# Performance work log

Hardware: AMD Instinct MI355X
Metric: run time of the kernel (lower is better)

Reference implementation:

```python
import jax, jax.numpy as jnp
import numpy as np
from jax import lax

B, T, K = 64, 2048, 128


def setup_inputs() -> dict:
    key = jax.random.key(0)
    k0, k1, k2, k3, k4, k5 = jax.random.split(key, 6)
    emissions = jax.random.normal(k0, (B, T, K), dtype=jnp.float32)
    lengths = jax.random.randint(k1, (B,), T // 2, T + 1)
    mask = jnp.arange(T)[None, :] < lengths[:, None]  # left-aligned [B,T] bool
    target = jax.random.bernoulli(k2, 0.5, (B, T, K))  # supervision set [B,T,K] bool
    forbidden_transitions = jax.random.bernoulli(k3, 0.1, (K, K))
    transitions = jax.random.normal(k4, (K, K), dtype=jnp.float32) * 0.01
    start_transitions = jax.random.normal(k5, (K,), dtype=jnp.float32) * 0.01
    return dict(emissions=emissions, mask=mask, target=target,
                transitions=transitions, start_transitions=start_transitions,
                forbidden_transitions=forbidden_transitions)


def reference(emissions, mask, target, transitions, start_transitions, forbidden_transitions):
    # Faithful to torch forward: transitions masked with -10000; end_transitions unused;
    # raw (unmasked) start_transitions added to EVERY timestep (as in the source).
    trans = jnp.where(forbidden_transitions, jnp.float32(-10000.0), transitions)  # [K,K]
    sup_em = jnp.where(target, emissions, jnp.float32(-100000.0))  # masked_fill(~target)
    bi = jnp.concatenate([sup_em, emissions], axis=0)  # [2B,T,K]
    bi = bi + start_transitions  # broadcast over all timesteps (source quirk)

    alpha0 = bi[:, 0]  # [2B,K]

    def step(alpha, em_t):
        # logdotexp: logsumexp_i(alpha[:,i] + trans[i,j]) + em_t[:,j]
        new = jax.nn.logsumexp(alpha[:, :, None] + trans[None, :, :], axis=1) + em_t
        return new, new

    _, outs = lax.scan(step, alpha0, jnp.swapaxes(bi[:, 1:], 0, 1))  # [T-1,2B,K]
    outs = jnp.concatenate([alpha0[None], outs], axis=0)  # [T,2B,K]

    lengths = mask.sum(-1)  # [B]
    last = jnp.concatenate([lengths, lengths]) - 1  # [2B]
    z_alpha = outs[last, jnp.arange(2 * B)]  # alpha at last valid step, [2B,K]
    z = jax.nn.logsumexp(z_alpha, axis=-1)  # [2B]
    supervised_z = z[:B]
    unsupervised_z = z[B:]
    return supervised_z - unsupervised_z
```

## Files before the change

### kernel.cpp

```cpp
#include <hip/hip_runtime.h>
#include <stdint.h>

#define BB 64
#define TT 2048
#define KK 128
#define CH 32

typedef float f32x16 __attribute__((ext_vector_type(16)));
typedef float f32x2  __attribute__((ext_vector_type(2)));

__device__ __forceinline__ float waveMax(float v) {
#pragma unroll
    for (int off = 32; off; off >>= 1) v = fmaxf(v, __shfl_xor(v, off, 64));
    return v;
}
__device__ __forceinline__ float waveSum(float v) {
#pragma unroll
    for (int off = 32; off; off >>= 1) v += __shfl_xor(v, off, 64);
    return v;
}
__device__ __forceinline__ int waveSumI(int v) {
#pragma unroll
    for (int off = 32; off; off >>= 1) v += __shfl_xor(v, off, 64);
    return v;
}
__device__ __forceinline__ float quadSum(float s) {
    int x = __builtin_amdgcn_mov_dpp(__float_as_int(s), 0xB1, 0xf, 0xf, true);
    s += __int_as_float(x);
    x = __builtin_amdgcn_mov_dpp(__float_as_int(s), 0x4E, 0xf, 0xf, true);
    s += __int_as_float(x);
    return s;
}
__device__ __forceinline__ float waveMaxFast(float v) {
    int x = __builtin_amdgcn_mov_dpp(__float_as_int(v), 0xB1, 0xf, 0xf, true);
    v = fmaxf(v, __int_as_float(x));
    x = __builtin_amdgcn_mov_dpp(__float_as_int(v), 0x4E, 0xf, 0xf, true);
    v = fmaxf(v, __int_as_float(x));
#pragma unroll
    for (int off = 4; off <= 32; off <<= 1) v = fmaxf(v, __shfl_xor(v, off, 64));
    return v;
}

template<int C> __device__ __forceinline__ float dppMax(float v) {
    int x = __builtin_amdgcn_mov_dpp(__float_as_int(v), C, 0xf, 0xf, true);
    return fmaxf(v, __int_as_float(x));
}
__device__ __forceinline__ float waveMaxTo63(float v) {
    v = dppMax<0xB1>(v);
    v = dppMax<0x4E>(v);
    v = dppMax<0x124>(v);
    v = dppMax<0x128>(v);
    v = dppMax<0x142>(v);
    v = dppMax<0x143>(v);
    return v;
}

__device__ __forceinline__ void lds_barrier() {
    asm volatile("s_waitcnt lgkmcnt(0)\n\ts_barrier" ::: "memory");
}

#define PKFMA(ep, wp, acc) acc = __builtin_elementwise_fma(ep, wp, acc)

#define MATVEC_QUARTER(Wa, Wb, ev, sOut) {                          \
    const float4 e0 = ev[0], e1 = ev[1], e2 = ev[2], e3 = ev[3];    \
    const float4 e4 = ev[4], e5 = ev[5], e6 = ev[6], e7 = ev[7];    \
    f32x2 a0 = {0.f,0.f}, a1 = {0.f,0.f}, a2 = {0.f,0.f}, a3 = {0.f,0.f}; \
    PKFMA(((f32x2){e0.x, e0.y}), ((f32x2){Wa[0],  Wa[1]}),  a0);    \
    PKFMA(((f32x2){e0.z, e0.w}), ((f32x2){Wa[2],  Wa[3]}),  a1);    \
    PKFMA(((f32x2){e1.x, e1.y}), ((f32x2){Wa[4],  Wa[5]}),  a2);    \
    PKFMA(((f32x2){e1.z, e1.w}), ((f32x2){Wa[6],  Wa[7]}),  a3);    \
    PKFMA(((f32x2){e2.x, e2.y}), ((f32x2){Wa[8],  Wa[9]}),  a0);    \
    PKFMA(((f32x2){e2.z, e2.w}), ((f32x2){Wa[10], Wa[11]}), a1);    \
    PKFMA(((f32x2){e3.x, e3.y}), ((f32x2){Wa[12], Wa[13]}), a2);    \
    PKFMA(((f32x2){e3.z, e3.w}), ((f32x2){Wa[14], Wa[15]}), a3);    \
    PKFMA(((f32x2){e4.x, e4.y}), ((f32x2){Wb[0],  Wb[1]}),  a0);    \
    PKFMA(((f32x2){e4.z, e4.w}), ((f32x2){Wb[2],  Wb[3]}),  a1);    \
    PKFMA(((f32x2){e5.x, e5.y}), ((f32x2){Wb[4],  Wb[5]}),  a2);    \
    PKFMA(((f32x2){e5.z, e5.w}), ((f32x2){Wb[6],  Wb[7]}),  a3);    \
    PKFMA(((f32x2){e6.x, e6.y}), ((f32x2){Wb[8],  Wb[9]}),  a0);    \
    PKFMA(((f32x2){e6.z, e6.w}), ((f32x2){Wb[10], Wb[11]}), a1);    \
    PKFMA(((f32x2){e7.x, e7.y}), ((f32x2){Wb[12], Wb[13]}), a2);    \
    PKFMA(((f32x2){e7.z, e7.w}), ((f32x2){Wb[14], Wb[15]}), a3);    \
    const f32x2 s2 = (a0 + a1) + (a2 + a3);                         \
    sOut = s2[0] + s2[1]; }

#define W_LIST(X) \
    X(0)  X(1)  X(2)  X(3)  X(4)  X(5)  X(6)  X(7)  \
    X(8)  X(9)  X(10) X(11) X(12) X(13) X(14) X(15) \
    X(16) X(17) X(18) X(19) X(20) X(21) X(22) X(23) \
    X(24) X(25) X(26) X(27) X(28) X(29) X(30) X(31) \
    X(32) X(33) X(34) X(35) X(36) X(37) X(38) X(39) \
    X(40) X(41) X(42) X(43) X(44) X(45) X(46) X(47) \
    X(48) X(49) X(50) X(51) X(52) X(53) X(54) X(55) \
    X(56) X(57) X(58) X(59) X(60) X(61) X(62) X(63)

#define WDECL(j) f32x2 W_##j;
#define WINIT_F(j) W_##j = (f32x2){ \
    forb[(2*(j)  )*KK + k] ? 0.0f : __expf(trans[(2*(j)  )*KK + k]), \
    forb[(2*(j)+1)*KK + k] ? 0.0f : __expf(trans[(2*(j)+1)*KK + k]) };
#define WINIT_B(j) W_##j = (f32x2){ \
    forb[k*KK + 2*(j)  ] ? 0.0f : __expf(trans[k*KK + 2*(j)  ]), \
    forb[k*KK + 2*(j)+1] ? 0.0f : __expf(trans[k*KK + 2*(j)+1]) };
#define WPIN(j) asm volatile("" : "+a"(W_##j));
#define WFMA(j, p0, p1, A0, A1) { const float4 E = ev[(j)]; \
    PKFMA(((f32x2){E.x, E.y}), W_##p0, A0); \
    PKFMA(((f32x2){E.z, E.w}), W_##p1, A1); }

extern "C" __global__ __launch_bounds__(128, 1)
__attribute__((amdgpu_waves_per_eu(1, 1)))
void crf_fb_kernel(const float* __restrict__ em,
                   const int* __restrict__ mask,
                   const int* __restrict__ tgt,
                   const float* __restrict__ trans,
                   const float* __restrict__ start,
                   const int* __restrict__ forb,
                   float* __restrict__ ef,
                   float* __restrict__ db,
                   float* __restrict__ Mfb)
{
    const int tid  = threadIdx.x;
    const int k    = tid;
    const int w    = tid >> 6;
    const int lane = tid & 63;
    const bool fwdDir = (blockIdx.x < 2 * BB);
    const int c    = blockIdx.x & (2 * BB - 1);
    const int b    = c & (BB - 1);
    const bool sup = (c < BB);

    __shared__ __align__(16) float biLDS[2][CH][KK];
    __shared__ __align__(16) float eLDS[2][KK];
    __shared__ __align__(8)  float wmLDS[2];
    __shared__ float redLDS[2];
    __shared__ int lenLDS;

    if (tid == 0) lenLDS = 0;
    int ps = 0;
    const int4* __restrict__ mrow = (const int4*)(mask + (size_t)b * TT);
#pragma unroll
    for (int it = 0; it < 4; ++it) {
        const int4 m4 = mrow[tid + 128 * it];
        ps += m4.x + m4.y + m4.z + m4.w;
    }
    ps = waveSumI(ps);
    __syncthreads();
    if (lane == 0) atomicAdd(&lenLDS, ps);

    const float st = start[k];
    const float* __restrict__ emrow = em + (size_t)b * TT * KK;
    const int* __restrict__ trow = tgt + (size_t)b * TT * KK;

    W_LIST(WDECL)
    if (fwdDir) {
        W_LIST(WINIT_F)
    } else {
        W_LIST(WINIT_B)
    }
    W_LIST(WPIN)
    __syncthreads();
    const int len = lenLDS;
    const int mid = len >> 1;
    const int N   = fwdDir ? mid : (len - 1 - mid);
    const int t0  = fwdDir ? 0 : (len - 1);

    float v0 = emrow[(size_t)t0 * KK + k];
    if (sup && !trow[(size_t)t0 * KK + k]) v0 = -100000.0f;
    v0 += st;
    const float wm0 = waveMax(v0);
    if (lane == 0) redLDS[w] = wm0;
    __syncthreads();
    const float M0 = fmaxf(redLDS[0], redLDS[1]);
    double M = (double)M0;
    float eNew = __expf(v0 - M0);
    eLDS[0][k] = eNew;

    const int scol = (tid & 31) << 2;
    const float4 stc = *(const float4*)(start + scol);
    auto stageChunk = [&](int bf, int m) {
        const int base_n = 1 + CH * m;
        const int t_base = fwdDir ? base_n : (len - base_n - CH);
#pragma unroll
        for (int i = 0; i < 8; ++i) {
            const int row = (tid >> 5) + (i << 2);
            const int t = t_base + row;
            float4 e4 = *(const float4*)(emrow + (size_t)t * KK + scol);
            if (sup) {
                const int4 t4 = *(const int4*)(trow + (size_t)t * KK + scol);
                e4.x = t4.x ? e4.x : -100000.0f;
                e4.y = t4.y ? e4.y : -100000.0f;
                e4.z = t4.z ? e4.z : -100000.0f;
                e4.w = t4.w ? e4.w : -100000.0f;
            }
            e4.x += stc.x; e4.y += stc.y; e4.z += stc.z; e4.w += stc.w;
            *(float4*)&biLDS[bf][row][scol] = e4;
        }
    };

    const int nChunks = (N + CH - 1) / CH;
    int buf = 0;
    stageChunk(0, 0);
    lds_barrier();

    for (int m = 0; m < nChunks; ++m) {
        if (m + 1 < nChunks) stageChunk(buf ^ 1, m + 1);
        const int base_n = 1 + CH * m;
        const int rem = N - base_n + 1;
        const int lim = rem < CH ? rem : CH;
#pragma unroll 4
        for (int i = 0; i < lim; ++i) {
            const int n = base_n + i;
            const int p = (n - 1) & 1;

            const int pos = fwdDir ? i : (CH - 1 - i);
            float bi = biLDS[buf][pos][k];
            if (!fwdDir && n == N) bi = 0.0f;

            if ((n & 3) == 3) {
                const float u = waveMaxTo63(__logf(eNew));
                if (lane == 63) wmLDS[w] = u;
            }
            float r = 0.0f;
            if ((n & 3) == 0) {
                const float2 wmv = *(const float2*)wmLDS;
                r = fmaxf(wmv.x, wmv.y);
                M += (double)r;
            }
            const float f = __expf(bi - r);

            const float4* __restrict__ ev = (const float4*)eLDS[p];
            f32x2 a0 = {0.f,0.f}, a1 = {0.f,0.f}, a2 = {0.f,0.f}, a3 = {0.f,0.f};
            WFMA( 0,  0,  1, a0, a1) WFMA( 1,  2,  3, a2, a3)
            WFMA( 2,  4,  5, a0, a1) WFMA( 3,  6,  7, a2, a3)
            WFMA( 4,  8,  9, a0, a1) WFMA( 5, 10, 11, a2, a3)
            WFMA( 6, 12, 13, a0, a1) WFMA( 7, 14, 15, a2, a3)
            WFMA( 8, 16, 17, a0, a1) WFMA( 9, 18, 19, a2, a3)
            WFMA(10, 20, 21, a0, a1) WFMA(11, 22, 23, a2, a3)
            WFMA(12, 24, 25, a0, a1) WFMA(13, 26, 27, a2, a3)
            WFMA(14, 28, 29, a0, a1) WFMA(15, 30, 31, a2, a3)
            WFMA(16, 32, 33, a0, a1) WFMA(17, 34, 35, a2, a3)
            WFMA(18, 36, 37, a0, a1) WFMA(19, 38, 39, a2, a3)
            WFMA(20, 40, 41, a0, a1) WFMA(21, 42, 43, a2, a3)
            WFMA(22, 44, 45, a0, a1) WFMA(23, 46, 47, a2, a3)
            WFMA(24, 48, 49, a0, a1) WFMA(25, 50, 51, a2, a3)
            WFMA(26, 52, 53, a0, a1) WFMA(27, 54, 55, a2, a3)
            WFMA(28, 56, 57, a0, a1) WFMA(29, 58, 59, a2, a3)
            WFMA(30, 60, 61, a0, a1) WFMA(31, 62, 63, a2, a3)
            const f32x2 aa = (a0 + a1) + (a2 + a3);
            const float s = aa[0] + aa[1];

            eNew = s * f;
            eLDS[p ^ 1][k] = eNew;

            lds_barrier();
        }
        buf ^= 1;
    }

    (fwdDir ? ef : db)[(size_t)c * KK + k] = eNew;
    if (tid == 0) Mfb[(fwdDir ? 0 : 2 * BB) + c] = (float)M;
}

extern "C" __global__ void crf_combine_kernel(const float* __restrict__ ef,
                                              const float* __restrict__ db,
                                              const float* __restrict__ Mfb,
                                              float* __restrict__ out)
{
    const int b = blockIdx.x;
    const int tid = threadIdx.x;
    const int wv = tid >> 6, lane = tid & 63;
    __shared__ float red[2][2];
    __shared__ float z[2];
#pragma unroll
    for (int s = 0; s < 2; ++s) {
        const int c = b + s * BB;
        const float v = ef[(size_t)c * KK + tid] * db[(size_t)c * KK + tid];
        const float p = waveSum(v);
        if (lane == 0) red[s][wv] = p;
    }
    __syncthreads();
    if (tid < 2) {
        const int c = b + tid * BB;
        z[tid] = Mfb[c] + Mfb[2 * BB + c] + __logf(red[tid][0] + red[tid][1]);
    }
    __syncthreads();
    if (tid == 0) out[b] = z[0] - z[1];
}

extern "C" __global__ __launch_bounds__(512)
__attribute__((amdgpu_waves_per_eu(2, 2)))
void crf_chain_kernel(const float* __restrict__ em, const int* __restrict__ mask,
                      const int* __restrict__ tgt, const float* __restrict__ trans,
                      const float* __restrict__ start, const int* __restrict__ forb,
                      float* __restrict__ zbuf)
{
    const int tid = threadIdx.x;
    const int k = tid >> 2, q = tid & 3, w = tid >> 6, lane = tid & 63;
    const int c = blockIdx.x, b = c & (BB - 1);
    const bool sup = (c < BB);
    __shared__ __align__(16) float eLDS[2][KK];
    __shared__ float wmLDS[8];
    __shared__ float redLDS[8];
    __shared__ int lenLDS;
    if (tid == 0) lenLDS = 0;
    const int4 m4 = ((const int4*)(mask + (size_t)b * TT))[tid];
    int ps = m4.x + m4.y + m4.z + m4.w;
    ps = waveSumI(ps);
    __syncthreads();
    if (lane == 0) atomicAdd(&lenLDS, ps);
    const float st = start[k];
    const float* __restrict__ emrow = em + (size_t)b * TT * KK;
    const int* __restrict__ trow = tgt + (size_t)b * TT * KK;
    const int ib = q * 32;
    f32x16 Wa, Wb;
#pragma unroll
    for (int j = 0; j < 16; ++j) {
        Wa[j] = forb[(ib + j     ) * KK + k] ? 0.0f : __expf(trans[(ib + j     ) * KK + k]);
        Wb[j] = forb[(ib + 16 + j) * KK + k] ? 0.0f : __expf(trans[(ib + 16 + j) * KK + k]);
    }
    float v0 = emrow[k];
    if (sup && !trow[k]) v0 = -100000.0f;
    v0 += st;
    const float wm0 = waveMax(v0);
    if (lane == 0) redLDS[w] = wm0;
    __syncthreads();
    const int len = lenLDS;
    float M0 = fmaxf(fmaxf(fmaxf(redLDS[0], redLDS[1]), fmaxf(redLDS[2], redLDS[3])),
                     fmaxf(fmaxf(redLDS[4], redLDS[5]), fmaxf(redLDS[6], redLDS[7])));
    double M = (double)M0;
    float eNew = __expf(v0 - M0);
    if (q == 0) eLDS[0][k] = eNew;
    auto bival = [&](int t) -> float {
        float e0 = emrow[(size_t)t * KK + k];
        if (sup) { if (!trow[(size_t)t * KK + k]) e0 = -100000.0f; }
        return e0 + st;
    };
    float biA = (len > 1) ? bival(1) : 0.0f;
    float biB = (len > 2) ? bival(2) : 0.0f;
    float biC = (len > 3) ? bival(3) : 0.0f;
    float biD = (len > 4) ? bival(4) : 0.0f;
    float sPrev = 1.0f, baPrev = 0.0f;
    lds_barrier();
#pragma unroll 4
    for (int t = 1; t < len; ++t) {
        const int p = (t - 1) & 1;
        const float biN = (t + 4 < len) ? bival(t + 4) : 0.0f;
        if ((t & 3) == 3) {
            const float u = __logf(sPrev) + baPrev;
            const float wmx = waveMaxFast(u);
            if (lane == 0) wmLDS[w] = wmx;
        }
        float r = 0.0f;
        if ((t & 3) == 0) {
            r = fmaxf(fmaxf(fmaxf(wmLDS[0], wmLDS[1]), fmaxf(wmLDS[2], wmLDS[3])),
                      fmaxf(fmaxf(wmLDS[4], wmLDS[5]), fmaxf(wmLDS[6], wmLDS[7])));
            M += (double)r;
        }
        const float ba = biA - r;
        const float f = __expf(ba);
        const float4* __restrict__ ev = (const float4*)eLDS[p] + q * 8;
        float s;
        MATVEC_QUARTER(Wa, Wb, ev, s)
        s = quadSum(s);
        eNew = s * f;
        if (q == 0) eLDS[p ^ 1][k] = eNew;
        sPrev = s; baPrev = ba;
        biA = biB; biB = biC; biC = biD; biD = biN;
        lds_barrier();
    }
    const float sm = waveSum((q == 0) ? eNew : 0.0f);
    if (lane == 0) redLDS[w] = sm;
    __syncthreads();
    if (tid == 0) {
        const float ss = ((redLDS[0] + redLDS[1]) + (redLDS[2] + redLDS[3]))
                       + ((redLDS[4] + redLDS[5]) + (redLDS[6] + redLDS[7]));
        zbuf[c] = (float)(M + (double)__logf(ss));
    }
}

extern "C" __global__ void crf_final_kernel(const float* __restrict__ z,
                                            float* __restrict__ out)
{
    const int b = threadIdx.x;
    out[b] = z[b] - z[b + BB];
}

extern "C" void kernel_launch(void* const* d_in, const int* in_sizes, int n_in,
                              void* d_out, int out_size, void* d_ws, size_t ws_size,
                              hipStream_t stream) {
    const float* em    = (const float*)d_in[0];
    const int*   mask  = (const int*)d_in[1];
    const int*   tgt   = (const int*)d_in[2];
    const float* trans = (const float*)d_in[3];
    const float* start = (const float*)d_in[4];
    const int*   forb  = (const int*)d_in[5];

    const size_t need = (size_t)(2 * 2 * BB * KK + 4 * BB) * sizeof(float);
    if (ws_size >= need) {
        float* ef  = (float*)d_ws;
        float* db  = ef + 2 * BB * KK;
        float* Mfb = db + 2 * BB * KK;
        crf_fb_kernel<<<4 * BB, 128, 0, stream>>>(em, mask, tgt, trans, start,
                                                  forb, ef, db, Mfb);
        crf_combine_kernel<<<BB, 128, 0, stream>>>(ef, db, Mfb, (float*)d_out);
    } else {
        float* zbuf = (float*)d_ws;
        crf_chain_kernel<<<2 * BB, 512, 0, stream>>>(em, mask, tgt, trans, start,
                                                     forb, zbuf);
        crf_final_kernel<<<1, BB, 0, stream>>>(zbuf, (float*)d_out);
    }
}
```

Baseline: 819.1 us.

## Run each CRF chain in a single wave with two states per lane

The forward/backward chain kernel drops from two waves to a single 64-lane wave per block, with each lane owning two consecutive states and holding both transition columns pinned in AGPRs. Within one wave the per-step barriers and the cross-wave LDS max exchange can go: the running max is computed with an in-wave DPP/shuffle reduction and the new alphas are written to and read from LDS by the same wave. In exchange each lane now does twice the packed FMAs per step on the serial critical path and uses roughly twice the register storage for weights. The chunk loop also has its unroll factors retuned.

```diff
diff --git a/kernel.cpp b/kernel.cpp
--- a/kernel.cpp
+++ b/kernel.cpp
@@ -38,20 +38,6 @@
     v = fmaxf(v, __int_as_float(x));
 #pragma unroll
     for (int off = 4; off <= 32; off <<= 1) v = fmaxf(v, __shfl_xor(v, off, 64));
-    return v;
-}
-
-template<int C> __device__ __forceinline__ float dppMax(float v) {
-    int x = __builtin_amdgcn_mov_dpp(__float_as_int(v), C, 0xf, 0xf, true);
-    return fmaxf(v, __int_as_float(x));
-}
-__device__ __forceinline__ float waveMaxTo63(float v) {
-    v = dppMax<0xB1>(v);
-    v = dppMax<0x4E>(v);
-    v = dppMax<0x124>(v);
-    v = dppMax<0x128>(v);
-    v = dppMax<0x142>(v);
-    v = dppMax<0x143>(v);
     return v;
 }
 
@@ -94,19 +80,26 @@
     X(48) X(49) X(50) X(51) X(52) X(53) X(54) X(55) \
     X(56) X(57) X(58) X(59) X(60) X(61) X(62) X(63)
 
-#define WDECL(j) f32x2 W_##j;
-#define WINIT_F(j) W_##j = (f32x2){ \
-    forb[(2*(j)  )*KK + k] ? 0.0f : __expf(trans[(2*(j)  )*KK + k]), \
-    forb[(2*(j)+1)*KK + k] ? 0.0f : __expf(trans[(2*(j)+1)*KK + k]) };
-#define WINIT_B(j) W_##j = (f32x2){ \
-    forb[k*KK + 2*(j)  ] ? 0.0f : __expf(trans[k*KK + 2*(j)  ]), \
-    forb[k*KK + 2*(j)+1] ? 0.0f : __expf(trans[k*KK + 2*(j)+1]) };
-#define WPIN(j) asm volatile("" : "+a"(W_##j));
-#define WFMA(j, p0, p1, A0, A1) { const float4 E = ev[(j)]; \
-    PKFMA(((f32x2){E.x, E.y}), W_##p0, A0); \
-    PKFMA(((f32x2){E.z, E.w}), W_##p1, A1); }
-
-extern "C" __global__ __launch_bounds__(128, 1)
+#define WDECL(j) f32x2 WA_##j, WB_##j;
+#define WINITPIN_F(j) \
+    WA_##j = (f32x2){ forb[(2*(j)  )*KK + k0] ? 0.0f : __expf(trans[(2*(j)  )*KK + k0]), \
+                      forb[(2*(j)+1)*KK + k0] ? 0.0f : __expf(trans[(2*(j)+1)*KK + k0]) }; \
+    WB_##j = (f32x2){ forb[(2*(j)  )*KK + k1] ? 0.0f : __expf(trans[(2*(j)  )*KK + k1]), \
+                      forb[(2*(j)+1)*KK + k1] ? 0.0f : __expf(trans[(2*(j)+1)*KK + k1]) }; \
+    asm volatile("" : "+a"(WA_##j), "+a"(WB_##j));
+#define WINITPIN_B(j) \
+    WA_##j = (f32x2){ forb[k0*KK + 2*(j)  ] ? 0.0f : __expf(trans[k0*KK + 2*(j)  ]), \
+                      forb[k0*KK + 2*(j)+1] ? 0.0f : __expf(trans[k0*KK + 2*(j)+1]) }; \
+    WB_##j = (f32x2){ forb[k1*KK + 2*(j)  ] ? 0.0f : __expf(trans[k1*KK + 2*(j)  ]), \
+                      forb[k1*KK + 2*(j)+1] ? 0.0f : __expf(trans[k1*KK + 2*(j)+1]) }; \
+    asm volatile("" : "+a"(WA_##j), "+a"(WB_##j));
+#define WF(j, a, b) { const float4 E = ev[(j)]; \
+    PKFMA(((f32x2){E.x, E.y}), WA_##a, A0); \
+    PKFMA(((f32x2){E.z, E.w}), WA_##b, A0b); \
+    PKFMA(((f32x2){E.x, E.y}), WB_##a, A1); \
+    PKFMA(((f32x2){E.z, E.w}), WB_##b, A1b); }
+
+extern "C" __global__ __launch_bounds__(64, 1)
 __attribute__((amdgpu_waves_per_eu(1, 1)))
 void crf_fb_kernel(const float* __restrict__ em,
                    const int* __restrict__ mask,
@@ -118,10 +111,9 @@
                    float* __restrict__ db,
                    float* __restrict__ Mfb)
 {
-    const int tid  = threadIdx.x;
-    const int k    = tid;
-    const int w    = tid >> 6;
-    const int lane = tid & 63;
+    const int lane = threadIdx.x;
+    const int k0   = lane << 1;
+    const int k1   = k0 + 1;
     const bool fwdDir = (blockIdx.x < 2 * BB);
     const int c    = blockIdx.x & (2 * BB - 1);
     const int b    = c & (BB - 1);
@@ -129,58 +121,52 @@
 
     __shared__ __align__(16) float biLDS[2][CH][KK];
     __shared__ __align__(16) float eLDS[2][KK];
-    __shared__ __align__(8)  float wmLDS[2];
-    __shared__ float redLDS[2];
-    __shared__ int lenLDS;
-
-    if (tid == 0) lenLDS = 0;
+
     int ps = 0;
     const int4* __restrict__ mrow = (const int4*)(mask + (size_t)b * TT);
 #pragma unroll
-    for (int it = 0; it < 4; ++it) {
-        const int4 m4 = mrow[tid + 128 * it];
+    for (int it = 0; it < 8; ++it) {
+        const int4 m4 = mrow[lane + 64 * it];
         ps += m4.x + m4.y + m4.z + m4.w;
     }
-    ps = waveSumI(ps);
-    __syncthreads();
-    if (lane == 0) atomicAdd(&lenLDS, ps);
-
-    const float st = start[k];
+    const int len = waveSumI(ps);
+
     const float* __restrict__ emrow = em + (size_t)b * TT * KK;
     const int* __restrict__ trow = tgt + (size_t)b * TT * KK;
 
     W_LIST(WDECL)
     if (fwdDir) {
-        W_LIST(WINIT_F)
+        W_LIST(WINITPIN_F)
     } else {
-        W_LIST(WINIT_B)
-    }
-    W_LIST(WPIN)
-    __syncthreads();
-    const int len = lenLDS;
+        W_LIST(WINITPIN_B)
+    }
+
     const int mid = len >> 1;
     const int N   = fwdDir ? mid : (len - 1 - mid);
     const int t0  = fwdDir ? 0 : (len - 1);
 
-    float v0 = emrow[(size_t)t0 * KK + k];
-    if (sup && !trow[(size_t)t0 * KK + k]) v0 = -100000.0f;
-    v0 += st;
-    const float wm0 = waveMax(v0);
-    if (lane == 0) redLDS[w] = wm0;
-    __syncthreads();
-    const float M0 = fmaxf(redLDS[0], redLDS[1]);
+    float2 v0 = *(const float2*)(emrow + (size_t)t0 * KK + k0);
+    if (sup) {
+        const int2 t2 = *(const int2*)(trow + (size_t)t0 * KK + k0);
+        v0.x = t2.x ? v0.x : -100000.0f;
+        v0.y = t2.y ? v0.y : -100000.0f;
+    }
+    const float2 st2 = *(const float2*)(start + k0);
+    v0.x += st2.x; v0.y += st2.y;
+    const float M0 = waveMaxFast(fmaxf(v0.x, v0.y));
     double M = (double)M0;
-    float eNew = __expf(v0 - M0);
-    eLDS[0][k] = eNew;
-
-    const int scol = (tid & 31) << 2;
+    float eNew0 = __expf(v0.x - M0);
+    float eNew1 = __expf(v0.y - M0);
+    *(f32x2*)&eLDS[0][k0] = (f32x2){eNew0, eNew1};
+
+    const int scol = (lane & 31) << 2;
     const float4 stc = *(const float4*)(start + scol);
     auto stageChunk = [&](int bf, int m) {
         const int base_n = 1 + CH * m;
         const int t_base = fwdDir ? base_n : (len - base_n - CH);
-#pragma unroll
-        for (int i = 0; i < 8; ++i) {
-            const int row = (tid >> 5) + (i << 2);
+#pragma unroll 4
+        for (int pss = 0; pss < 16; ++pss) {
+            const int row = (pss << 1) + (lane >> 5);
             const int t = t_base + row;
             float4 e4 = *(const float4*)(emrow + (size_t)t * KK + scol);
             if (sup) {
@@ -198,65 +184,53 @@
     const int nChunks = (N + CH - 1) / CH;
     int buf = 0;
     stageChunk(0, 0);
-    lds_barrier();
+    float rPend = 0.0f;
 
     for (int m = 0; m < nChunks; ++m) {
         if (m + 1 < nChunks) stageChunk(buf ^ 1, m + 1);
         const int base_n = 1 + CH * m;
         const int rem = N - base_n + 1;
         const int lim = rem < CH ? rem : CH;
-#pragma unroll 4
+#pragma unroll 2
         for (int i = 0; i < lim; ++i) {
             const int n = base_n + i;
             const int p = (n - 1) & 1;
-
             const int pos = fwdDir ? i : (CH - 1 - i);
-            float bi = biLDS[buf][pos][k];
-            if (!fwdDir && n == N) bi = 0.0f;
+
+            float2 bi = *(const float2*)&biLDS[buf][pos][k0];
+            if (!fwdDir && n == N) { bi.x = 0.0f; bi.y = 0.0f; }
 
             if ((n & 3) == 3) {
-                const float u = waveMaxTo63(__logf(eNew));
-                if (lane == 63) wmLDS[w] = u;
+                rPend = waveMaxFast(__logf(fmaxf(eNew0, eNew1)));
             }
             float r = 0.0f;
-            if ((n & 3) == 0) {
-                const float2 wmv = *(const float2*)wmLDS;
-                r = fmaxf(wmv.x, wmv.y);
-                M += (double)r;
-            }
-            const float f = __expf(bi - r);
+            if ((n & 3) == 0) { r = rPend; M += (double)r; }
+            const float f0 = __expf(bi.x - r);
+            const float f1 = __expf(bi.y - r);
 
             const float4* __restrict__ ev = (const float4*)eLDS[p];
-            f32x2 a0 = {0.f,0.f}, a1 = {0.f,0.f}, a2 = {0.f,0.f}, a3 = {0.f,0.f};
-            WFMA( 0,  0,  1, a0, a1) WFMA( 1,  2,  3, a2, a3)
-            WFMA( 2,  4,  5, a0, a1) WFMA( 3,  6,  7, a2, a3)
-            WFMA( 4,  8,  9, a0, a1) WFMA( 5, 10, 11, a2, a3)
-            WFMA( 6, 12, 13, a0, a1) WFMA( 7, 14, 15, a2, a3)
-            WFMA( 8, 16, 17, a0, a1) WFMA( 9, 18, 19, a2, a3)
-            WFMA(10, 20, 21, a0, a1) WFMA(11, 22, 23, a2, a3)
-            WFMA(12, 24, 25, a0, a1) WFMA(13, 26, 27, a2, a3)
-            WFMA(14, 28, 29, a0, a1) WFMA(15, 30, 31, a2, a3)
-            WFMA(16, 32, 33, a0, a1) WFMA(17, 34, 35, a2, a3)
-            WFMA(18, 36, 37, a0, a1) WFMA(19, 38, 39, a2, a3)
-            WFMA(20, 40, 41, a0, a1) WFMA(21, 42, 43, a2, a3)
-            WFMA(22, 44, 45, a0, a1) WFMA(23, 46, 47, a2, a3)
-            WFMA(24, 48, 49, a0, a1) WFMA(25, 50, 51, a2, a3)
-            WFMA(26, 52, 53, a0, a1) WFMA(27, 54, 55, a2, a3)
-            WFMA(28, 56, 57, a0, a1) WFMA(29, 58, 59, a2, a3)
-            WFMA(30, 60, 61, a0, a1) WFMA(31, 62, 63, a2, a3)
-            const f32x2 aa = (a0 + a1) + (a2 + a3);
-            const float s = aa[0] + aa[1];
-
-            eNew = s * f;
-            eLDS[p ^ 1][k] = eNew;
-
-            lds_barrier();
+            f32x2 A0 = {0.f,0.f}, A0b = {0.f,0.f};
+            f32x2 A1 = {0.f,0.f}, A1b = {0.f,0.f};
+            WF( 0,  0,  1) WF( 1,  2,  3) WF( 2,  4,  5) WF( 3,  6,  7)
+            WF( 4,  8,  9) WF( 5, 10, 11) WF( 6, 12, 13) WF( 7, 14, 15)
+            WF( 8, 16, 17) WF( 9, 18, 19) WF(10, 20, 21) WF(11, 22, 23)
+            WF(12, 24, 25) WF(13, 26, 27) WF(14, 28, 29) WF(15, 30, 31)
+            WF(16, 32, 33) WF(17, 34, 35) WF(18, 36, 37) WF(19, 38, 39)
+            WF(20, 40, 41) WF(21, 42, 43) WF(22, 44, 45) WF(23, 46, 47)
+            WF(24, 48, 49) WF(25, 50, 51) WF(26, 52, 53) WF(27, 54, 55)
+            WF(28, 56, 57) WF(29, 58, 59) WF(30, 60, 61) WF(31, 62, 63)
+            const f32x2 s0v = A0 + A0b;
+            const f32x2 s1v = A1 + A1b;
+            eNew0 = (s0v[0] + s0v[1]) * f0;
+            eNew1 = (s1v[0] + s1v[1]) * f1;
+            *(f32x2*)&eLDS[p ^ 1][k0] = (f32x2){eNew0, eNew1};
         }
         buf ^= 1;
     }
 
-    (fwdDir ? ef : db)[(size_t)c * KK + k] = eNew;
-    if (tid == 0) Mfb[(fwdDir ? 0 : 2 * BB) + c] = (float)M;
+    float* __restrict__ dst = (fwdDir ? ef : db) + (size_t)c * KK;
+    *(f32x2*)&dst[k0] = (f32x2){eNew0, eNew1};
+    if (lane == 0) Mfb[(fwdDir ? 0 : 2 * BB) + c] = (float)M;
 }
 
 extern "C" __global__ void crf_combine_kernel(const float* __restrict__ ef,
@@ -398,8 +372,8 @@
         float* ef  = (float*)d_ws;
         float* db  = ef + 2 * BB * KK;
         float* Mfb = db + 2 * BB * KK;
-        crf_fb_kernel<<<4 * BB, 128, 0, stream>>>(em, mask, tgt, trans, start,
-                                                  forb, ef, db, Mfb);
+        crf_fb_kernel<<<4 * BB, 64, 0, stream>>>(em, mask, tgt, trans, start,
+                                                 forb, ef, db, Mfb);
         crf_combine_kernel<<<BB, 128, 0, stream>>>(ef, db, Mfb, (float*)d_out);
     } else {
         float* zbuf = (float*)d_ws;
```

After: 1.712 ms. 2.09x slower.
